# Optimization experiments

Hardware: AMD Instinct MI355X
Metric: run time of the kernel (lower is better)

## Reference

```python
import jax, jax.numpy as jnp
import numpy as np

B, C, R, M, N = 8, 16, 16, 512, 512
ASYM = 1e-3


def _rot(a, z):
    # torch: r = (a*z).diff(-1) = a1*z1 - a0*z0 ; i = (a*z[...,[1,0]]).sum(-1) = a0*z1 + a1*z0
    r = a[..., 1] * z[..., 1] - a[..., 0] * z[..., 0]
    i = a[..., 0] * z[..., 1] + a[..., 1] * z[..., 0]
    return jnp.stack([r, i], axis=-1)


def _cmatmul(a, b):
    # complex matmul on trailing [..., P, Q, 2] x [..., Q, S, 2] (equivalent to the A/B einsum trick)
    ar, ai = a[..., 0], a[..., 1]
    br, bi = b[..., 0], b[..., 1]
    return jnp.stack([ar @ br - ai @ bi, ar @ bi + ai @ br], axis=-1)


def setup_inputs() -> dict:
    key = jax.random.key(0)
    ks = jax.random.split(key, 14)
    rn = lambda k, s, sc=1.0: jax.random.normal(k, s, dtype=jnp.float32) * sc
    rot_init = lambda k1, k2: jnp.concatenate(
        [1.0 + rn(k1, (1, C, 1, 1, 1), ASYM), rn(k2, (1, C, 1, 1, 1), ASYM)], axis=-1)
    return {
        "x": rn(ks[0], (B, C)),
        "weights_i": rn(ks[1], (1, 1, M, M, 2), 1.0 / np.log(M * M)),
        "weights_j": rn(ks[2], (1, 1, N, N, 2), 1.0 / np.log(N * N)),
        "weights_base": rn(ks[3], (1, 1, M, N, 2), 1.0 / np.log(M * N)),
        "translate_base": rn(ks[4], (1, C, 1, 1, 2), ASYM),
        "rotate_base": rot_init(ks[5], ks[6]),
        "translate_dynamic": rn(ks[7], (1, C, 1, 1, 2), ASYM),
        "rotate_dynamic": rot_init(ks[8], ks[9]),
        "mod_i": rn(ks[10], (1, C, R, M, 2), 1.0 / np.log(R * M)),
        "mod_j": rn(ks[11], (1, C, R, N, 2)),
        "inversions": -1.0 + rn(ks[12], (1, C, 1, 1, 2), ASYM),
        "mod_transforms": rn(ks[13], (4, C, 2 * C), np.sqrt(2.0 / (3 * C))),
    }


def reference(x, weights_i, weights_j, weights_base, translate_base, rotate_base,
              translate_dynamic, rotate_dynamic, mod_i, mod_j, inversions, mod_transforms):
    Bx = x.shape[0]
    # NOTE: the original computes a rotated/translated `weights` from weights_base,
    # translate_base, rotate_base that is never used afterwards (dead code) -> omitted.
    t = jnp.einsum('bc,kcl->bkl', x, mod_transforms)          # [B,4,2C]
    t = t.reshape(Bx, 4, C, 1, 1, 2)
    # low-rank modulation factors, per component, rotated by dynamic transforms
    mi = _rot(mod_i + t[:, 0], t[:, 1])                        # [B,C,R,M,2]
    mj = _rot(mod_j + t[:, 2], t[:, 3])                        # [B,C,R,N,2]
    # inversion-rotate mod_i then sum over components
    mi = _rot(mi, inversions).sum(axis=1, keepdims=True)       # [B,1,R,M,2]
    # "division-like" inversion for mod_j then sum over components
    denom = (mj * mj).sum(axis=-1, keepdims=True)
    r = (inversions * mj).sum(axis=-1, keepdims=True) / denom
    i = (inversions[..., 0:1] * mj[..., 1:2] - inversions[..., 1:2] * mj[..., 0:1]) / denom
    mj = jnp.concatenate([r, i], axis=-1).sum(axis=1, keepdims=True)  # [B,1,R,N,2]
    # complex outer-product modulation: [B,1,M,R] @ [B,1,R,N] -> [B,1,M,N,2]
    mod = _cmatmul(jnp.swapaxes(mi, -3, -2), mj)
    mr = mod[..., 0]
    mr = (mr - mr.mean(axis=(-2, -1), keepdims=True)) / jnp.std(mr, axis=(-2, -1), ddof=1, keepdims=True)
    mod = jnp.stack([mr, mod[..., 1]], axis=-1)
    # modulate base weights (componentwise, not complex mult)
    wd = weights_base + weights_base * mod                     # [B,1,M,N,2]
    # cross-mixing complex matmuls
    wd = _cmatmul(jnp.swapaxes(wd, -3, -2), weights_i)         # [B,1,N,M,2]
    wd = _cmatmul(jnp.swapaxes(wd, -3, -2), weights_j)         # [B,1,M,N,2]
    # per-component dynamic translate + rotate, sum components, take real part
    wd = wd + translate_dynamic                                # [B,C,M,N,2]
    wd = _rot(wd, rotate_dynamic).sum(axis=1)[..., 0]          # [B,M,N]
    return wd
```

## Files before the change

kernel.cpp:

```cpp
#include <hip/hip_runtime.h>
#include <hip/hip_bf16.h>
#include <math.h>


#define WS_T       0
#define WS_DE      1024
#define WS_SCAL    1280
#define WS_STATS   1296
#define WS_PART    1536
#define WS_MIS     4096
#define WS_MJS     135168
#define WS_BASET   266240
#define WS_A2      790528
#define WS_B5T     1052672
#define WS_MODT    1314816
#define WS_G1X     1314816
#define WS_B2T     5509120

typedef __attribute__((ext_vector_type(8))) short short8;
typedef __attribute__((ext_vector_type(4))) float f32x4;

__device__ __forceinline__ unsigned short f2bf(float f) {
    unsigned int u = __float_as_uint(f);
    u = (u + 0x7FFFu + ((u >> 16) & 1u)) >> 16;
    return (unsigned short)u;
}
__device__ __forceinline__ unsigned int pack2bf(float a, float b) {
    return (unsigned int)f2bf(a) | ((unsigned int)f2bf(b) << 16);
}
__device__ __forceinline__ void load_lds16(const unsigned int* g, unsigned short* l) {
    __builtin_amdgcn_global_load_lds((const __attribute__((address_space(1))) unsigned int*)g,
                                     (__attribute__((address_space(3))) unsigned int*)l, 16, 0, 0);
}

__global__ void k_prep(const float* __restrict__ x, const float* __restrict__ mt,
                       const float* __restrict__ inv, const float* __restrict__ td,
                       const float* __restrict__ rd, float* __restrict__ ws) {
    float* tbuf = ws + WS_T;
    float* de   = ws + WS_DE;
    float* scal = ws + WS_SCAL;
    int tid = threadIdx.x;
    for (int i = tid; i < 1024; i += 256) {
        int b = i >> 7, k = (i >> 5) & 3, l = i & 31;
        float s = 0.f;
        for (int c = 0; c < 16; c++) s += x[b * 16 + c] * mt[(k * 16 + c) * 32 + l];
        tbuf[i] = s;
    }
    __syncthreads();
    if (tid < 128) {
        int b = tid >> 4, c = tid & 15;
        float i0 = inv[2 * c], i1 = inv[2 * c + 1];
        float z0 = tbuf[(b * 4 + 1) * 32 + 2 * c], z1 = tbuf[(b * 4 + 1) * 32 + 2 * c + 1];
        de[tid * 2]     = i0 * z0 + i1 * z1;
        de[tid * 2 + 1] = i0 * z1 - i1 * z0;
    }
    if (tid == 0) {
        float S0 = 0.f, S1 = 0.f, CCv = 0.f;
        for (int c = 0; c < 16; c++) {
            float r0 = rd[2 * c], r1 = rd[2 * c + 1];
            float t0 = td[2 * c], t1 = td[2 * c + 1];
            S0 += r0; S1 += r1;
            CCv += t1 * r1 - t0 * r0;
        }
        scal[0] = -S0; scal[1] = -S1; scal[2] = CCv;
    }
}

__global__ void k_trans(const float* __restrict__ Wi, const float* __restrict__ Wj,
                        const float* __restrict__ base, float* __restrict__ ws) {
    __shared__ float2 tile[32][33];
    int mode = blockIdx.z;
    int bx = blockIdx.x, by = blockIdx.y;
    int tx = threadIdx.x & 31, ty = threadIdx.x >> 5;
    const float* src = (mode == 0) ? Wi : (mode == 1) ? Wj : base;
    for (int i = 0; i < 4; i++) {
        int rIn = by * 32 + ty + i * 8;
        int cIn = bx * 32 + tx;
        tile[ty + i * 8][tx] = *(const float2*)(src + ((size_t)rIn * 512 + cIn) * 2);
    }
    __syncthreads();
    if (mode == 0) {
        unsigned int* A2u = (unsigned int*)(ws + WS_A2);
        for (int i = 0; i < 4; i++) {
            int rOut = bx * 32 + ty + i * 8;
            int cOut = by * 32 + tx;
            float2 v = tile[tx][ty + i * 8];
            A2u[(size_t)rOut * 512 + cOut] = pack2bf(v.x, v.y);
        }
    } else if (mode == 1) {
        const float* scal = ws + WS_SCAL;
        float ar = scal[0], ai = scal[1];
        unsigned int* B5u = (unsigned int*)(ws + WS_B5T);
        for (int i = 0; i < 4; i++) {
            int rOut = bx * 32 + ty + i * 8;
            int cOut = by * 32 + tx;
            float2 v = tile[tx][ty + i * 8];
            float wr = ar * v.x - ai * v.y;
            float wi = ar * v.y + ai * v.x;
            B5u[(size_t)rOut * 512 + cOut] = pack2bf(wr, -wi);
        }
    } else {
        float* baseT = ws + WS_BASET;
        for (int i = 0; i < 4; i++) {
            int rOut = bx * 32 + ty + i * 8;
            int cOut = by * 32 + tx;
            *(float2*)(baseT + ((size_t)rOut * 512 + cOut) * 2) = tile[tx][ty + i * 8];
        }
    }
}

__global__ void k_mi(const float* __restrict__ mod_i, float* __restrict__ ws) {
    const float* tbuf = ws + WS_T;
    const float* de   = ws + WS_DE;
    float* mi_s       = ws + WS_MIS;
    int id = blockIdx.x * 256 + threadIdx.x;
    int b = id >> 13, rm = id & 8191;
    int r = rm >> 9, m = rm & 511;
    float acc0 = 0.f, acc1 = 0.f;
    for (int c = 0; c < 16; c++) {
        const float* p = mod_i + (((size_t)(c * 16 + r) * 512) + m) * 2;
        float t00 = tbuf[(b * 4 + 0) * 32 + 2 * c];
        float t01 = tbuf[(b * 4 + 0) * 32 + 2 * c + 1];
        float d = de[(b * 16 + c) * 2], e = de[(b * 16 + c) * 2 + 1];
        float A0 = p[0] + t00, A1 = p[1] + t01;
        acc0 += d * A0 - e * A1;
        acc1 += e * A0 + d * A1;
    }
    float* dst = mi_s + ((size_t)b * 8192 + rm) * 2;
    dst[0] = acc0; dst[1] = acc1;
}

__global__ void k_mj(const float* __restrict__ mod_j, const float* __restrict__ inv,
                     float* __restrict__ ws) {
    const float* tbuf = ws + WS_T;
    float* mj_s       = ws + WS_MJS;
    int id = blockIdx.x * 256 + threadIdx.x;
    int b = id >> 13, rn = id & 8191;
    int r = rn >> 9, n = rn & 511;
    float acc0 = 0.f, acc1 = 0.f;
    for (int c = 0; c < 16; c++) {
        const float* p = mod_j + (((size_t)(c * 16 + r) * 512) + n) * 2;
        float t20 = tbuf[(b * 4 + 2) * 32 + 2 * c];
        float t21 = tbuf[(b * 4 + 2) * 32 + 2 * c + 1];
        float z0  = tbuf[(b * 4 + 3) * 32 + 2 * c];
        float z1  = tbuf[(b * 4 + 3) * 32 + 2 * c + 1];
        float A0 = p[0] + t20, A1 = p[1] + t21;
        float w0 = -z0 * A0 + z1 * A1;
        float w1 =  z1 * A0 + z0 * A1;
        float i0 = inv[2 * c], i1 = inv[2 * c + 1];
        float den = w0 * w0 + w1 * w1;
        acc0 += (i0 * w0 + i1 * w1) / den;
        acc1 += (i0 * w1 - i1 * w0) / den;
    }
    float* dst = mj_s + ((size_t)b * 8192 + rn) * 2;
    dst[0] = acc0; dst[1] = acc1;
}

__global__ __launch_bounds__(256) void k_modT(float* __restrict__ ws) {
    const float* mi_s = ws + WS_MIS;
    const float* mj_s = ws + WS_MJS;
    float* modT       = ws + WS_MODT;
    float* partials   = ws + WS_PART;
    int mt = blockIdx.x, nt = blockIdx.y, b = blockIdx.z;
    __shared__ float Ns[16][128];
    __shared__ float Ms[16][128];
    __shared__ float red[512];
    int tid = threadIdx.x, tx = tid & 15, ty = tid >> 4;
    const float* Nb = mj_s + (size_t)b * 16384;
    const float* Mb = mi_s + (size_t)b * 16384;
    int n0 = nt * 64, m0 = mt * 64;
    for (int i = 0; i < 4; i++) {
        int flat = tid + i * 256;
        int col = flat & 63, r = flat >> 6;
        float2 sa = *(const float2*)(Nb + ((size_t)r * 512 + n0 + col) * 2);
        Ns[r][col * 2] = sa.x; Ns[r][col * 2 + 1] = sa.y;
        float2 sb = *(const float2*)(Mb + ((size_t)r * 512 + m0 + col) * 2);
        Ms[r][col * 2] = sb.x; Ms[r][col * 2 + 1] = sb.y;
    }
    __syncthreads();
    float cr[4][4] = {}, ci[4][4] = {};
    for (int r = 0; r < 16; r++) {
        float nr[4], ni[4], mr[4], mi_[4];
        for (int i = 0; i < 4; i++) { nr[i] = Ns[r][(ty * 4 + i) * 2]; ni[i] = Ns[r][(ty * 4 + i) * 2 + 1]; }
        for (int j = 0; j < 4; j++) { mr[j] = Ms[r][(tx * 4 + j) * 2]; mi_[j] = Ms[r][(tx * 4 + j) * 2 + 1]; }
        for (int i = 0; i < 4; i++)
            for (int j = 0; j < 4; j++) {
                cr[i][j] += nr[i] * mr[j] - ni[i] * mi_[j];
                ci[i][j] += nr[i] * mi_[j] + ni[i] * mr[j];
            }
    }
    float s1 = 0.f, s2 = 0.f;
    float* ob = modT + (size_t)b * 524288;
    for (int i = 0; i < 4; i++) {
        float* dst = ob + ((size_t)(n0 + ty * 4 + i) * 512 + m0 + tx * 4) * 2;
        for (int j = 0; j < 4; j++) {
            dst[j * 2] = cr[i][j]; dst[j * 2 + 1] = ci[i][j];
            s1 += cr[i][j]; s2 += cr[i][j] * cr[i][j];
        }
    }
    red[tid] = s1; red[256 + tid] = s2;
    __syncthreads();
    for (int s = 128; s > 0; s >>= 1) {
        if (tid < s) { red[tid] += red[tid + s]; red[256 + tid] += red[256 + tid + s]; }
        __syncthreads();
    }
    if (tid == 0) {
        float* dst = partials + ((size_t)b * 64 + nt * 8 + mt) * 2;
        dst[0] = red[0]; dst[1] = red[256];
    }
}

__global__ void k_stats(float* __restrict__ ws) {
    const float* partials = ws + WS_PART;
    float* stats          = ws + WS_STATS;
    __shared__ float s1[512], s2[512];
    int tid = threadIdx.x;
    int b = tid >> 6, i = tid & 63;
    s1[tid] = partials[(b * 64 + i) * 2];
    s2[tid] = partials[(b * 64 + i) * 2 + 1];
    __syncthreads();
    for (int s = 32; s > 0; s >>= 1) {
        if (i < s) { s1[tid] += s1[tid + s]; s2[tid] += s2[tid + s]; }
        __syncthreads();
    }
    if (i == 0) {
        double MN = 262144.0;
        double mu = (double)s1[tid] / MN;
        double var = ((double)s2[tid] - MN * mu * mu) / (MN - 1.0);
        if (var < 1e-30) var = 1e-30;
        stats[b * 2] = (float)mu;
        stats[b * 2 + 1] = (float)(1.0 / sqrt(var));
    }
}

__global__ void k_wd0(float* __restrict__ ws) {
    const float* stats = ws + WS_STATS;
    const float* modT  = ws + WS_MODT;
    const float* baseT = ws + WS_BASET;
    unsigned int* B2T  = (unsigned int*)(ws + WS_B2T);
    int id = blockIdx.x * 256 + threadIdx.x;
    int b = id >> 18, nm = id & 262143;
    int n = nm >> 9, m = nm & 511;
    float mu = stats[b * 2], rstd = stats[b * 2 + 1];
    float2 mv = *(const float2*)(modT + ((size_t)b * 262144 + nm) * 2);
    float2 bs = *(const float2*)(baseT + (size_t)nm * 2);
    float wr = bs.x * (1.f + (mv.x - mu) * rstd);
    float wi = bs.y * (1.f + mv.y);
    unsigned int* Bb = B2T + (size_t)b * 524288;
    Bb[(size_t)(2 * n) * 512 + m]     = pack2bf(wr, -wi);
    Bb[(size_t)(2 * n + 1) * 512 + m] = pack2bf(wi, wr);
}

template <int NGL, bool OUT_BF16>
__global__ __launch_bounds__(256) void k_gemm(const unsigned short* __restrict__ Aall,
                                              const unsigned short* __restrict__ BTall,
                                              void* __restrict__ Call,
                                              const float* __restrict__ scal,
                                              size_t a_bs, size_t bt_bs, size_t c_bs) {
    constexpr int K = 1024;
    __shared__ __align__(16) unsigned short As[128 * 64];
    __shared__ __align__(16) unsigned short Bs[128 * 64];
    const int tid = threadIdx.x;
    const int b = blockIdx.z;
    const unsigned short* A  = Aall  + (size_t)b * a_bs;
    const unsigned short* BT = BTall + (size_t)b * bt_bs;
    const int mBase = blockIdx.y * 128;
    const int nBase = blockIdx.x * 128;
    const int wave = tid >> 6, lane = tid & 63;
    const int wm = wave >> 1, wn = wave & 1;
    const int l15 = lane & 15, q = lane >> 4;

    f32x4 acc[4][4];
    for (int i = 0; i < 4; i++)
        for (int j = 0; j < 4; j++) acc[i][j] = (f32x4)0.f;

    const int flat0 = tid;
    for (int k0 = 0; k0 < K; k0 += 64) {
#pragma unroll
        for (int p = 0; p < 4; p++) {
            int flat = flat0 + p * 256;
            int r = flat >> 3, c = flat & 7;
            int gc = ((c ^ (r & 7)) << 3);
            load_lds16((const unsigned int*)(A + (size_t)(mBase + r) * K + k0 + gc),
                       &As[flat << 3]);
            load_lds16((const unsigned int*)(BT + (size_t)(nBase + r) * K + k0 + gc),
                       &Bs[flat << 3]);
        }
        __syncthreads();
#pragma unroll
        for (int ks = 0; ks < 2; ks++) {
            short8 af[4], bfr[4];
#pragma unroll
            for (int t = 0; t < 4; t++) {
                int ra = wm * 64 + t * 16 + l15;
                int ja = (ks * 4 + q) ^ (ra & 7);
                af[t] = *(const short8*)&As[ra * 64 + ja * 8];
                int rb = wn * 64 + t * 16 + l15;
                int jb = (ks * 4 + q) ^ (rb & 7);
                bfr[t] = *(const short8*)&Bs[rb * 64 + jb * 8];
            }
#pragma unroll
            for (int i = 0; i < 4; i++)
#pragma unroll
                for (int j = 0; j < 4; j++)
                    acc[i][j] = __builtin_amdgcn_mfma_f32_16x16x32_bf16(af[i], bfr[j], acc[i][j], 0, 0, 0);
        }
        __syncthreads();
    }

    if constexpr (OUT_BF16) {
        __shared__ __align__(16) unsigned short Cs[128 * 132];
#pragma unroll
        for (int i = 0; i < 4; i++) {
            int row0 = wm * 64 + i * 16 + q * 4;
#pragma unroll
            for (int j = 0; j < 4; j++) {
                int col = wn * 64 + j * 16 + l15;
#pragma unroll
                for (int r = 0; r < 4; r++)
                    Cs[(row0 + r) * 132 + col] = f2bf(acc[i][j][r]);
            }
        }
        __syncthreads();
        unsigned short* C = (unsigned short*)Call + (size_t)b * c_bs;
#pragma unroll
        for (int p = 0; p < 8; p++) {
            int flat = tid + p * 256;
            int r = flat >> 4, c = flat & 15;
            short8 v = *(const short8*)&Cs[r * 132 + c * 8];
            *(short8*)(C + (size_t)(mBase + r) * NGL + nBase + c * 8) = v;
        }
    } else {
        float CC = scal[2];
        float* C = (float*)Call + (size_t)b * c_bs;
#pragma unroll
        for (int i = 0; i < 4; i++) {
            int row0 = wm * 64 + i * 16 + q * 4;
#pragma unroll
            for (int j = 0; j < 4; j++) {
                int col = wn * 64 + j * 16 + l15;
#pragma unroll
                for (int r = 0; r < 4; r++)
                    C[(size_t)(mBase + row0 + r) * NGL + nBase + col] = acc[i][j][r] + CC;
            }
        }
    }
}

extern "C" void kernel_launch(void* const* d_in, const int* in_sizes, int n_in,
                              void* d_out, int out_size, void* d_ws, size_t ws_size,
                              hipStream_t stream) {
    const float* x    = (const float*)d_in[0];
    const float* Wi   = (const float*)d_in[1];
    const float* Wj   = (const float*)d_in[2];
    const float* base = (const float*)d_in[3];
    const float* td   = (const float*)d_in[6];
    const float* rd   = (const float*)d_in[7];
    const float* modi = (const float*)d_in[8];
    const float* modj = (const float*)d_in[9];
    const float* inv  = (const float*)d_in[10];
    const float* mt   = (const float*)d_in[11];
    float* ws  = (float*)d_ws;
    float* out = (float*)d_out;

    unsigned short* A2  = (unsigned short*)(ws + WS_A2);
    unsigned short* B5T = (unsigned short*)(ws + WS_B5T);
    unsigned short* B2T = (unsigned short*)(ws + WS_B2T);
    unsigned short* G1X = (unsigned short*)(ws + WS_G1X);
    const float* scal   = ws + WS_SCAL;

    k_prep<<<1, 256, 0, stream>>>(x, mt, inv, td, rd, ws);
    k_trans<<<dim3(16, 16, 3), 256, 0, stream>>>(Wi, Wj, base, ws);
    k_mi<<<256, 256, 0, stream>>>(modi, ws);
    k_mj<<<256, 256, 0, stream>>>(modj, inv, ws);
    k_modT<<<dim3(8, 8, 8), 256, 0, stream>>>(ws);
    k_stats<<<1, 512, 0, stream>>>(ws);
    k_wd0<<<8192, 256, 0, stream>>>(ws);
    k_gemm<1024, true><<<dim3(8, 4, 8), 256, 0, stream>>>(
        A2, B2T, (void*)G1X, scal, (size_t)0, (size_t)1048576, (size_t)524288);
    k_gemm<512, false><<<dim3(4, 4, 8), 256, 0, stream>>>(
        G1X, B5T, (void*)out, scal, (size_t)524288, (size_t)0, (size_t)262144);
}
```

Measured before the change: 157.6 us.

## Compute modulation stats via Gram matrices, fuse modT into B2T build, retile GEMMs

Merges the mi and mj kernels into one launch. The mean and variance of the modulation's real part are now computed analytically from 16x16 Gram matrices of the rank-R factors, so the full modT tensor and its separate reduction kernels are no longer materialised. The outer-product kernel now writes the normalized, modulated bf16 B2T operand directly, which drops the k_wd0 pass and the modT round trip through memory. Both GEMMs are retiled to 64-row tiles so they launch more blocks, with only one operand staged in LDS and the other read straight from global memory. The risks are a tiny 8-block Gram kernel on the critical path, possible float cancellation in the variance formula, and uncoalesced direct global operand loads.

After: 178.9 us. 13.5% more time.

```diff
diff --git a/kernel.cpp b/kernel.cpp
--- a/kernel.cpp
+++ b/kernel.cpp
@@ -7,15 +7,13 @@
 #define WS_DE      1024
 #define WS_SCAL    1280
 #define WS_STATS   1296
-#define WS_PART    1536
 #define WS_MIS     4096
 #define WS_MJS     135168
 #define WS_BASET   266240
 #define WS_A2      790528
 #define WS_B5T     1052672
-#define WS_MODT    1314816
 #define WS_G1X     1314816
-#define WS_B2T     5509120
+#define WS_B2T     3411968
 
 typedef __attribute__((ext_vector_type(8))) short short8;
 typedef __attribute__((ext_vector_type(4))) float f32x4;
@@ -109,62 +107,110 @@
     }
 }
 
-__global__ void k_mi(const float* __restrict__ mod_i, float* __restrict__ ws) {
+__global__ void k_mimj(const float* __restrict__ mod_i, const float* __restrict__ mod_j,
+                       const float* __restrict__ inv, float* __restrict__ ws) {
     const float* tbuf = ws + WS_T;
-    const float* de   = ws + WS_DE;
-    float* mi_s       = ws + WS_MIS;
-    int id = blockIdx.x * 256 + threadIdx.x;
-    int b = id >> 13, rm = id & 8191;
-    int r = rm >> 9, m = rm & 511;
-    float acc0 = 0.f, acc1 = 0.f;
-    for (int c = 0; c < 16; c++) {
-        const float* p = mod_i + (((size_t)(c * 16 + r) * 512) + m) * 2;
-        float t00 = tbuf[(b * 4 + 0) * 32 + 2 * c];
-        float t01 = tbuf[(b * 4 + 0) * 32 + 2 * c + 1];
-        float d = de[(b * 16 + c) * 2], e = de[(b * 16 + c) * 2 + 1];
-        float A0 = p[0] + t00, A1 = p[1] + t01;
-        acc0 += d * A0 - e * A1;
-        acc1 += e * A0 + d * A1;
-    }
-    float* dst = mi_s + ((size_t)b * 8192 + rm) * 2;
-    dst[0] = acc0; dst[1] = acc1;
-}
-
-__global__ void k_mj(const float* __restrict__ mod_j, const float* __restrict__ inv,
-                     float* __restrict__ ws) {
-    const float* tbuf = ws + WS_T;
-    float* mj_s       = ws + WS_MJS;
-    int id = blockIdx.x * 256 + threadIdx.x;
-    int b = id >> 13, rn = id & 8191;
-    int r = rn >> 9, n = rn & 511;
-    float acc0 = 0.f, acc1 = 0.f;
-    for (int c = 0; c < 16; c++) {
-        const float* p = mod_j + (((size_t)(c * 16 + r) * 512) + n) * 2;
-        float t20 = tbuf[(b * 4 + 2) * 32 + 2 * c];
-        float t21 = tbuf[(b * 4 + 2) * 32 + 2 * c + 1];
-        float z0  = tbuf[(b * 4 + 3) * 32 + 2 * c];
-        float z1  = tbuf[(b * 4 + 3) * 32 + 2 * c + 1];
-        float A0 = p[0] + t20, A1 = p[1] + t21;
-        float w0 = -z0 * A0 + z1 * A1;
-        float w1 =  z1 * A0 + z0 * A1;
-        float i0 = inv[2 * c], i1 = inv[2 * c + 1];
-        float den = w0 * w0 + w1 * w1;
-        acc0 += (i0 * w0 + i1 * w1) / den;
-        acc1 += (i0 * w1 - i1 * w0) / den;
-    }
-    float* dst = mj_s + ((size_t)b * 8192 + rn) * 2;
-    dst[0] = acc0; dst[1] = acc1;
-}
-
-__global__ __launch_bounds__(256) void k_modT(float* __restrict__ ws) {
-    const float* mi_s = ws + WS_MIS;
-    const float* mj_s = ws + WS_MJS;
-    float* modT       = ws + WS_MODT;
-    float* partials   = ws + WS_PART;
+    int blk = blockIdx.x;
+    if (blk < 256) {
+        const float* de = ws + WS_DE;
+        float* mi_s     = ws + WS_MIS;
+        int id = blk * 256 + threadIdx.x;
+        int b = id >> 13, rm = id & 8191;
+        float acc0 = 0.f, acc1 = 0.f;
+        for (int c = 0; c < 16; c++) {
+            const float* p = mod_i + (((size_t)c * 8192) + rm) * 2;
+            float t00 = tbuf[(b * 4 + 0) * 32 + 2 * c];
+            float t01 = tbuf[(b * 4 + 0) * 32 + 2 * c + 1];
+            float d = de[(b * 16 + c) * 2], e = de[(b * 16 + c) * 2 + 1];
+            float A0 = p[0] + t00, A1 = p[1] + t01;
+            acc0 += d * A0 - e * A1;
+            acc1 += e * A0 + d * A1;
+        }
+        float* dst = mi_s + ((size_t)b * 8192 + rm) * 2;
+        dst[0] = acc0; dst[1] = acc1;
+    } else {
+        float* mj_s = ws + WS_MJS;
+        int id = (blk - 256) * 256 + threadIdx.x;
+        int b = id >> 13, rn = id & 8191;
+        float acc0 = 0.f, acc1 = 0.f;
+        for (int c = 0; c < 16; c++) {
+            const float* p = mod_j + (((size_t)c * 8192) + rn) * 2;
+            float t20 = tbuf[(b * 4 + 2) * 32 + 2 * c];
+            float t21 = tbuf[(b * 4 + 2) * 32 + 2 * c + 1];
+            float z0  = tbuf[(b * 4 + 3) * 32 + 2 * c];
+            float z1  = tbuf[(b * 4 + 3) * 32 + 2 * c + 1];
+            float A0 = p[0] + t20, A1 = p[1] + t21;
+            float w0 = -z0 * A0 + z1 * A1;
+            float w1 =  z1 * A0 + z0 * A1;
+            float i0 = inv[2 * c], i1 = inv[2 * c + 1];
+            float den = w0 * w0 + w1 * w1;
+            acc0 += (i0 * w0 + i1 * w1) / den;
+            acc1 += (i0 * w1 - i1 * w0) / den;
+        }
+        float* dst = mj_s + ((size_t)b * 8192 + rn) * 2;
+        dst[0] = acc0; dst[1] = acc1;
+    }
+}
+
+__global__ __launch_bounds__(256) void k_gram(float* __restrict__ ws) {
+    __shared__ float2 Vs[16][130];
+    __shared__ float2 Us[16][130];
+    int b = blockIdx.x, tid = threadIdx.x;
+    int r = tid >> 4, r2 = tid & 15;
+    const float2* V = (const float2*)(ws + WS_MIS + (size_t)b * 16384);
+    const float2* U = (const float2*)(ws + WS_MJS + (size_t)b * 16384);
+    float Svr = 0, Svi = 0, Tvr = 0, Tvi = 0;
+    float Sur = 0, Sui = 0, Tur = 0, Tui = 0;
+    float ar = 0, ai = 0, br = 0, bi = 0;
+    for (int h = 0; h < 4; h++) {
+        for (int p = 0; p < 8; p++) {
+            int f = tid + p * 256;
+            int rr = f >> 7, mm = f & 127;
+            Vs[rr][mm] = V[rr * 512 + h * 128 + mm];
+            Us[rr][mm] = U[rr * 512 + h * 128 + mm];
+        }
+        __syncthreads();
+        for (int mm = 0; mm < 128; mm++) {
+            float2 v1 = Vs[r][mm], v2 = Vs[r2][mm];
+            float2 u1 = Us[r][mm], u2 = Us[r2][mm];
+            Svr += v1.x * v2.x - v1.y * v2.y;  Svi += v1.x * v2.y + v1.y * v2.x;
+            Tvr += v1.x * v2.x + v1.y * v2.y;  Tvi += v1.y * v2.x - v1.x * v2.y;
+            Sur += u1.x * u2.x - u1.y * u2.y;  Sui += u1.x * u2.y + u1.y * u2.x;
+            Tur += u1.x * u2.x + u1.y * u2.y;  Tui += u1.y * u2.x - u1.x * u2.y;
+            if (r2 == 0) { ar += v1.x; ai += v1.y; br += u1.x; bi += u1.y; }
+        }
+        __syncthreads();
+    }
+    float val = (Sur * Svr - Sui * Svi) + (Tur * Tvr - Tui * Tvi);
+    float mterm = (r2 == 0) ? (br * ar - bi * ai) : 0.f;
+    float* red = (float*)&Vs[0][0];
+    red[tid] = val; red[256 + tid] = mterm;
+    __syncthreads();
+    for (int s = 128; s > 0; s >>= 1) {
+        if (tid < s) { red[tid] += red[tid + s]; red[256 + tid] += red[256 + tid + s]; }
+        __syncthreads();
+    }
+    if (tid == 0) {
+        double MN = 262144.0;
+        double mu = (double)red[256] / MN;
+        double sumsq = 0.5 * (double)red[0];
+        double var = (sumsq - MN * mu * mu) / (MN - 1.0);
+        if (var < 1e-30) var = 1e-30;
+        float* stats = ws + WS_STATS;
+        stats[b * 2] = (float)mu;
+        stats[b * 2 + 1] = (float)(1.0 / sqrt(var));
+    }
+}
+
+__global__ __launch_bounds__(256) void k_bmod(float* __restrict__ ws) {
+    const float* mi_s  = ws + WS_MIS;
+    const float* mj_s  = ws + WS_MJS;
+    const float* baseT = ws + WS_BASET;
+    const float* stats = ws + WS_STATS;
+    unsigned int* B2T  = (unsigned int*)(ws + WS_B2T);
     int mt = blockIdx.x, nt = blockIdx.y, b = blockIdx.z;
     __shared__ float Ns[16][128];
     __shared__ float Ms[16][128];
-    __shared__ float red[512];
     int tid = threadIdx.x, tx = tid & 15, ty = tid >> 4;
     const float* Nb = mj_s + (size_t)b * 16384;
     const float* Mb = mi_s + (size_t)b * 16384;
@@ -189,159 +235,135 @@
                 ci[i][j] += nr[i] * mi_[j] + ni[i] * mr[j];
             }
     }
-    float s1 = 0.f, s2 = 0.f;
-    float* ob = modT + (size_t)b * 524288;
+    float mu = stats[b * 2], rstd = stats[b * 2 + 1];
+    unsigned int* Bb = B2T + (size_t)b * 524288;
     for (int i = 0; i < 4; i++) {
-        float* dst = ob + ((size_t)(n0 + ty * 4 + i) * 512 + m0 + tx * 4) * 2;
+        int n = n0 + ty * 4 + i;
+        int mcol = m0 + tx * 4;
+        const float4* bsp = (const float4*)(baseT + ((size_t)n * 512 + mcol) * 2);
+        float4 b01 = bsp[0], b23 = bsp[1];
+        float bsr[4] = {b01.x, b01.z, b23.x, b23.z};
+        float bsi[4] = {b01.y, b01.w, b23.y, b23.w};
+        uint4 w0, w1;
+        unsigned int* p0 = (unsigned int*)&w0;
+        unsigned int* p1 = (unsigned int*)&w1;
         for (int j = 0; j < 4; j++) {
-            dst[j * 2] = cr[i][j]; dst[j * 2 + 1] = ci[i][j];
-            s1 += cr[i][j]; s2 += cr[i][j] * cr[i][j];
-        }
-    }
-    red[tid] = s1; red[256 + tid] = s2;
-    __syncthreads();
-    for (int s = 128; s > 0; s >>= 1) {
-        if (tid < s) { red[tid] += red[tid + s]; red[256 + tid] += red[256 + tid + s]; }
-        __syncthreads();
-    }
-    if (tid == 0) {
-        float* dst = partials + ((size_t)b * 64 + nt * 8 + mt) * 2;
-        dst[0] = red[0]; dst[1] = red[256];
-    }
-}
-
-__global__ void k_stats(float* __restrict__ ws) {
-    const float* partials = ws + WS_PART;
-    float* stats          = ws + WS_STATS;
-    __shared__ float s1[512], s2[512];
-    int tid = threadIdx.x;
-    int b = tid >> 6, i = tid & 63;
-    s1[tid] = partials[(b * 64 + i) * 2];
-    s2[tid] = partials[(b * 64 + i) * 2 + 1];
-    __syncthreads();
-    for (int s = 32; s > 0; s >>= 1) {
-        if (i < s) { s1[tid] += s1[tid + s]; s2[tid] += s2[tid + s]; }
-        __syncthreads();
-    }
-    if (i == 0) {
-        double MN = 262144.0;
-        double mu = (double)s1[tid] / MN;
-        double var = ((double)s2[tid] - MN * mu * mu) / (MN - 1.0);
-        if (var < 1e-30) var = 1e-30;
-        stats[b * 2] = (float)mu;
-        stats[b * 2 + 1] = (float)(1.0 / sqrt(var));
-    }
-}
-
-__global__ void k_wd0(float* __restrict__ ws) {
-    const float* stats = ws + WS_STATS;
-    const float* modT  = ws + WS_MODT;
-    const float* baseT = ws + WS_BASET;
-    unsigned int* B2T  = (unsigned int*)(ws + WS_B2T);
-    int id = blockIdx.x * 256 + threadIdx.x;
-    int b = id >> 18, nm = id & 262143;
-    int n = nm >> 9, m = nm & 511;
-    float mu = stats[b * 2], rstd = stats[b * 2 + 1];
-    float2 mv = *(const float2*)(modT + ((size_t)b * 262144 + nm) * 2);
-    float2 bs = *(const float2*)(baseT + (size_t)nm * 2);
-    float wr = bs.x * (1.f + (mv.x - mu) * rstd);
-    float wi = bs.y * (1.f + mv.y);
-    unsigned int* Bb = B2T + (size_t)b * 524288;
-    Bb[(size_t)(2 * n) * 512 + m]     = pack2bf(wr, -wi);
-    Bb[(size_t)(2 * n + 1) * 512 + m] = pack2bf(wi, wr);
-}
-
-template <int NGL, bool OUT_BF16>
+            float wr = bsr[j] * (1.f + (cr[i][j] - mu) * rstd);
+            float wi = bsi[j] * (1.f + ci[i][j]);
+            p0[j] = pack2bf(wr, -wi);
+            p1[j] = pack2bf(wi, wr);
+        }
+        *(uint4*)&Bb[(size_t)(2 * n) * 512 + mcol]     = w0;
+        *(uint4*)&Bb[(size_t)(2 * n + 1) * 512 + mcol] = w1;
+    }
+}
+
+template <int TN, bool STAGE_B, bool OUT_BF16>
 __global__ __launch_bounds__(256) void k_gemm(const unsigned short* __restrict__ Aall,
                                               const unsigned short* __restrict__ BTall,
                                               void* __restrict__ Call,
                                               const float* __restrict__ scal,
-                                              size_t a_bs, size_t bt_bs, size_t c_bs) {
+                                              size_t a_bs, size_t bt_bs, size_t c_bs,
+                                              int ngl) {
     constexpr int K = 1024;
-    __shared__ __align__(16) unsigned short As[128 * 64];
-    __shared__ __align__(16) unsigned short Bs[128 * 64];
+    constexpr int WJT = TN / 32;
+    constexpr int SROWS = STAGE_B ? TN : 64;
+    constexpr int SM1 = SROWS * 64;
+    constexpr int SM2 = OUT_BF16 ? 64 * 136 : 0;
+    constexpr int SMEMN = SM1 > SM2 ? SM1 : SM2;
+    __shared__ __align__(16) unsigned short smem[SMEMN];
+
     const int tid = threadIdx.x;
     const int b = blockIdx.z;
     const unsigned short* A  = Aall  + (size_t)b * a_bs;
     const unsigned short* BT = BTall + (size_t)b * bt_bs;
-    const int mBase = blockIdx.y * 128;
-    const int nBase = blockIdx.x * 128;
+    const unsigned short* Sg = STAGE_B ? BT : A;
+    const unsigned short* Dg = STAGE_B ? A  : BT;
+    const int mBase = blockIdx.y * 64;
+    const int nBase = blockIdx.x * TN;
+    const int sBase = STAGE_B ? nBase : mBase;
     const int wave = tid >> 6, lane = tid & 63;
     const int wm = wave >> 1, wn = wave & 1;
     const int l15 = lane & 15, q = lane >> 4;
 
-    f32x4 acc[4][4];
-    for (int i = 0; i < 4; i++)
-        for (int j = 0; j < 4; j++) acc[i][j] = (f32x4)0.f;
-
-    const int flat0 = tid;
+    f32x4 acc[2][WJT];
+    for (int i = 0; i < 2; i++)
+        for (int j = 0; j < WJT; j++) acc[i][j] = (f32x4)0.f;
+
     for (int k0 = 0; k0 < K; k0 += 64) {
 #pragma unroll
-        for (int p = 0; p < 4; p++) {
-            int flat = flat0 + p * 256;
+        for (int p = 0; p < SROWS * 8 / 256; p++) {
+            int flat = tid + p * 256;
             int r = flat >> 3, c = flat & 7;
-            int gc = ((c ^ (r & 7)) << 3);
-            load_lds16((const unsigned int*)(A + (size_t)(mBase + r) * K + k0 + gc),
-                       &As[flat << 3]);
-            load_lds16((const unsigned int*)(BT + (size_t)(nBase + r) * K + k0 + gc),
-                       &Bs[flat << 3]);
-        }
+            int gc = (c ^ (r & 7)) << 3;
+            load_lds16((const unsigned int*)(Sg + (size_t)(sBase + r) * K + k0 + gc),
+                       &smem[flat << 3]);
+        }
+        short8 df[2][2];
+#pragma unroll
+        for (int ks = 0; ks < 2; ks++)
+#pragma unroll
+            for (int t = 0; t < 2; t++) {
+                int row = STAGE_B ? (mBase + wm * 32 + t * 16 + l15)
+                                  : (nBase + wn * (TN / 2) + t * 16 + l15);
+                df[ks][t] = *(const short8*)(Dg + (size_t)row * K + k0 + (ks * 4 + q) * 8);
+            }
         __syncthreads();
 #pragma unroll
         for (int ks = 0; ks < 2; ks++) {
-            short8 af[4], bfr[4];
-#pragma unroll
-            for (int t = 0; t < 4; t++) {
-                int ra = wm * 64 + t * 16 + l15;
-                int ja = (ks * 4 + q) ^ (ra & 7);
-                af[t] = *(const short8*)&As[ra * 64 + ja * 8];
-                int rb = wn * 64 + t * 16 + l15;
-                int jb = (ks * 4 + q) ^ (rb & 7);
-                bfr[t] = *(const short8*)&Bs[rb * 64 + jb * 8];
+            constexpr int SN = STAGE_B ? WJT : 2;
+            short8 sf[SN];
+#pragma unroll
+            for (int t = 0; t < SN; t++) {
+                int sr = (STAGE_B ? wn * (TN / 2) : wm * 32) + t * 16 + l15;
+                int sj = (ks * 4 + q) ^ (sr & 7);
+                sf[t] = *(const short8*)&smem[sr * 64 + sj * 8];
             }
 #pragma unroll
-            for (int i = 0; i < 4; i++)
-#pragma unroll
-                for (int j = 0; j < 4; j++)
-                    acc[i][j] = __builtin_amdgcn_mfma_f32_16x16x32_bf16(af[i], bfr[j], acc[i][j], 0, 0, 0);
+            for (int i = 0; i < 2; i++)
+#pragma unroll
+                for (int j = 0; j < WJT; j++) {
+                    short8 af = STAGE_B ? df[ks][i] : sf[i];
+                    short8 bf = STAGE_B ? sf[j] : df[ks][j];
+                    acc[i][j] = __builtin_amdgcn_mfma_f32_16x16x32_bf16(af, bf, acc[i][j], 0, 0, 0);
+                }
         }
         __syncthreads();
     }
 
     if constexpr (OUT_BF16) {
-        __shared__ __align__(16) unsigned short Cs[128 * 132];
-#pragma unroll
-        for (int i = 0; i < 4; i++) {
-            int row0 = wm * 64 + i * 16 + q * 4;
-#pragma unroll
-            for (int j = 0; j < 4; j++) {
-                int col = wn * 64 + j * 16 + l15;
+#pragma unroll
+        for (int i = 0; i < 2; i++) {
+            int row0 = wm * 32 + i * 16 + q * 4;
+#pragma unroll
+            for (int j = 0; j < WJT; j++) {
+                int col = wn * (TN / 2) + j * 16 + l15;
 #pragma unroll
                 for (int r = 0; r < 4; r++)
-                    Cs[(row0 + r) * 132 + col] = f2bf(acc[i][j][r]);
+                    smem[(row0 + r) * 136 + col] = f2bf(acc[i][j][r]);
             }
         }
         __syncthreads();
         unsigned short* C = (unsigned short*)Call + (size_t)b * c_bs;
 #pragma unroll
-        for (int p = 0; p < 8; p++) {
+        for (int p = 0; p < TN / 32; p++) {
             int flat = tid + p * 256;
-            int r = flat >> 4, c = flat & 15;
-            short8 v = *(const short8*)&Cs[r * 132 + c * 8];
-            *(short8*)(C + (size_t)(mBase + r) * NGL + nBase + c * 8) = v;
+            int r = flat / (TN / 8), c = flat % (TN / 8);
+            short8 v = *(const short8*)&smem[r * 136 + c * 8];
+            *(short8*)(C + (size_t)(mBase + r) * ngl + nBase + c * 8) = v;
         }
     } else {
         float CC = scal[2];
         float* C = (float*)Call + (size_t)b * c_bs;
 #pragma unroll
-        for (int i = 0; i < 4; i++) {
-            int row0 = wm * 64 + i * 16 + q * 4;
-#pragma unroll
-            for (int j = 0; j < 4; j++) {
-                int col = wn * 64 + j * 16 + l15;
+        for (int i = 0; i < 2; i++) {
+            int row0 = mBase + wm * 32 + i * 16 + q * 4;
+#pragma unroll
+            for (int j = 0; j < WJT; j++) {
+                int col = nBase + wn * (TN / 2) + j * 16 + l15;
 #pragma unroll
                 for (int r = 0; r < 4; r++)
-                    C[(size_t)(mBase + row0 + r) * NGL + nBase + col] = acc[i][j][r] + CC;
+                    C[(size_t)(row0 + r) * ngl + col] = acc[i][j][r] + CC;
             }
         }
     }
@@ -371,13 +393,11 @@
 
     k_prep<<<1, 256, 0, stream>>>(x, mt, inv, td, rd, ws);
     k_trans<<<dim3(16, 16, 3), 256, 0, stream>>>(Wi, Wj, base, ws);
-    k_mi<<<256, 256, 0, stream>>>(modi, ws);
-    k_mj<<<256, 256, 0, stream>>>(modj, inv, ws);
-    k_modT<<<dim3(8, 8, 8), 256, 0, stream>>>(ws);
-    k_stats<<<1, 512, 0, stream>>>(ws);
-    k_wd0<<<8192, 256, 0, stream>>>(ws);
-    k_gemm<1024, true><<<dim3(8, 4, 8), 256, 0, stream>>>(
-        A2, B2T, (void*)G1X, scal, (size_t)0, (size_t)1048576, (size_t)524288);
-    k_gemm<512, false><<<dim3(4, 4, 8), 256, 0, stream>>>(
-        G1X, B5T, (void*)out, scal, (size_t)524288, (size_t)0, (size_t)262144);
-}
+    k_mimj<<<512, 256, 0, stream>>>(modi, modj, inv, ws);
+    k_gram<<<8, 256, 0, stream>>>(ws);
+    k_bmod<<<dim3(8, 8, 8), 256, 0, stream>>>(ws);
+    k_gemm<128, true, true><<<dim3(8, 8, 8), 256, 0, stream>>>(
+        A2, B2T, (void*)G1X, scal, (size_t)0, (size_t)1048576, (size_t)524288, 1024);
+    k_gemm<64, false, false><<<dim3(8, 8, 8), 256, 0, stream>>>(
+        G1X, B5T, (void*)out, scal, (size_t)524288, (size_t)0, (size_t)262144, 512);
+}
```
